# Kernel tuning notes

Hardware: AMD Instinct MI355X
Metric: run time of the kernel (lower is better)

## Reference

```python
import jax, jax.numpy as jnp
import numpy as np

B, T, D, H, L = 64, 4096, 128, 128, 2


def setup_inputs() -> dict:
    key = jax.random.key(0)
    ks = jax.random.split(key, 9)
    s = 1.0 / np.sqrt(H)
    return {
        "x": jax.random.normal(ks[0], (B, T, D), dtype=jnp.float32),
        "W_ih0": jax.random.normal(ks[1], (3 * H, D), dtype=jnp.float32) * s,
        "W_hh0": jax.random.normal(ks[2], (3 * H, H), dtype=jnp.float32) * s,
        "b_ih0": jax.random.normal(ks[3], (3 * H,), dtype=jnp.float32) * s,
        "b_hh0": jax.random.normal(ks[4], (3 * H,), dtype=jnp.float32) * s,
        "W_ih1": jax.random.normal(ks[5], (3 * H, H), dtype=jnp.float32) * s,
        "W_hh1": jax.random.normal(ks[6], (3 * H, H), dtype=jnp.float32) * s,
        "b_ih1": jax.random.normal(ks[7], (3 * H,), dtype=jnp.float32) * s,
        "b_hh1": jax.random.normal(ks[8], (3 * H,), dtype=jnp.float32) * s,
    }


def _gru_cell(h, xt, W_ih, W_hh, b_ih, b_hh):
    # torch.nn.GRUCell math; gates packed as [r, z, n] along 3H.
    gi = xt @ W_ih.T + b_ih            # [B, 3H]
    gh = h @ W_hh.T + b_hh             # [B, 3H]
    i_r, i_z, i_n = jnp.split(gi, 3, axis=-1)
    h_r, h_z, h_n = jnp.split(gh, 3, axis=-1)
    r = jax.nn.sigmoid(i_r + h_r)
    z = jax.nn.sigmoid(i_z + h_z)
    n = jnp.tanh(i_n + r * h_n)
    return (1.0 - z) * n + z * h


def reference(x, W_ih0, W_hh0, b_ih0, b_hh0, W_ih1, W_hh1, b_ih1, b_hh1):
    h0 = jnp.zeros((L, x.shape[0], H), dtype=x.dtype)
    params = ((W_ih0, W_hh0, b_ih0, b_hh0), (W_ih1, W_hh1, b_ih1, b_hh1))

    def step(h, xt):
        # h: [L, B, H]; xt: [B, D]
        inp = xt
        new_h = []
        for l in range(L):
            hl = _gru_cell(h[l], inp, *params[l])
            new_h.append(hl)
            inp = hl
        return jnp.stack(new_h, axis=0), None

    xs = jnp.swapaxes(x, 0, 1)  # [T, B, D]
    h_final, _ = jax.lax.scan(step, h0, xs)
    return h_final  # [L, B, H]
```

## Files before the change

### kernel.cpp

```cpp
#include <hip/hip_runtime.h>


#define Tlen 4096
#define Hd   128
#define Bsz  64

typedef __attribute__((ext_vector_type(8))) short short8;
typedef __attribute__((ext_vector_type(4))) short short4v;
typedef __attribute__((ext_vector_type(4))) float float4v;
typedef __attribute__((ext_vector_type(2))) unsigned int uint2v;

#define MFMA16(a, b, c) __builtin_amdgcn_mfma_f32_16x16x32_bf16((a), (b), (c), 0, 0, 0)

static __device__ __forceinline__ float fast_exp2(float x) {
#if __has_builtin(__builtin_amdgcn_exp2f)
  return __builtin_amdgcn_exp2f(x);
#else
  return exp2f(x);
#endif
}
static __device__ __forceinline__ float fast_rcp(float x) {
  return __builtin_amdgcn_rcpf(x);
}
static __device__ __forceinline__ short f2bf(float f) {
  unsigned u = __builtin_bit_cast(unsigned, f);
  u = (u + 0x7FFFu + ((u >> 16) & 1u)) >> 16;
  return (short)u;
}
static __device__ __forceinline__ unsigned pk2bf(float a, float b) {
#if __has_builtin(__builtin_amdgcn_cvt_pk_bf16_f32)
  auto v = __builtin_amdgcn_cvt_pk_bf16_f32(a, b);
  return __builtin_bit_cast(unsigned, v);
#else
  return (unsigned)(unsigned short)f2bf(a) | ((unsigned)(unsigned short)f2bf(b) << 16);
#endif
}
static __device__ __forceinline__ short8 loadw8(const float* __restrict__ p) {
  short8 r;
  #pragma unroll
  for (int j = 0; j < 8; ++j) r[j] = f2bf(p[j]);
  return r;
}

#define XB   0
#define H0B  4096
#define H1B  8192
#define BLK  2048

__global__ __launch_bounds__(512, 2) void gru_scan(
    const float* __restrict__ x,
    const float* __restrict__ Wih0, const float* __restrict__ Whh0,
    const float* __restrict__ bih0, const float* __restrict__ bhh0,
    const float* __restrict__ Wih1, const float* __restrict__ Whh1,
    const float* __restrict__ bih1, const float* __restrict__ bhh1,
    float* __restrict__ out) {
  __shared__ alignas(16) short Abuf[12288];

  const int tid   = threadIdx.x;
  const int wave  = tid >> 6;
  const int lane  = tid & 63;
  const int lc    = lane & 15;
  const int quad  = lane >> 4;
  const int q8    = quad * 8;
  const int lane8 = lane * 8;
  const int bbase = blockIdx.x * 16;

  const int wgrp = wave >> 2;
  const int w4   = wave & 3;

  const float* Wi = wgrp ? Wih1 : Wih0;
  const float* Wh = wgrp ? Whh1 : Whh0;
  const float* bi = wgrp ? bih1 : bih0;
  const float* bh = wgrp ? bhh1 : bhh0;

  short8 fxr[2][4], fxz[2][4], fxn[2][4];
  short8 fhr[2][4], fhz[2][4], fhn[2][4];
  float kr[2], kz[2], ki[2], kh[2];
  const float nL  = -1.44269504088896f;
  const float n2L = -2.88539008177793f;
  #pragma unroll
  for (int G = 0; G < 2; ++G) {
    const int c = 32 * w4 + 16 * G + lc;
    #pragma unroll
    for (int s = 0; s < 4; ++s) {
      const int k = 32 * s + q8;
      fxr[G][s] = loadw8(Wi + (c)       * Hd + k);
      fxz[G][s] = loadw8(Wi + (128 + c) * Hd + k);
      fxn[G][s] = loadw8(Wi + (256 + c) * Hd + k);
      fhr[G][s] = loadw8(Wh + (c)       * Hd + k);
      fhz[G][s] = loadw8(Wh + (128 + c) * Hd + k);
      fhn[G][s] = loadw8(Wh + (256 + c) * Hd + k);
    }
    kr[G] = nL  * (bi[c] + bh[c]);
    kz[G] = nL  * (bi[128 + c] + bh[128 + c]);
    ki[G] = n2L * bi[256 + c];
    kh[G] = n2L * bh[256 + c];
  }

  const int hsel = wgrp ? H1B : H0B;
  const int isel = wgrp ? H0B : XB;

  int hw[2];
  #pragma unroll
  for (int G = 0; G < 2; ++G)
    hw[G] = w4 * 512 + (2 * G + (lc >> 3)) * 128 + (lc & 7);

  const int xrow = tid >> 5;
  const int xk0  = 4 * (tid & 31);
  const int xwoff = (xk0 >> 5) * 512 + ((xk0 >> 3) & 3) * 128 + xrow * 8 + (xk0 & 7);
  const float* xg = x + (size_t)(bbase + xrow) * (Tlen * Hd) + xk0;

  const int glo = wgrp ? 2 : 0;
  const int ghi = glo + Tlen;

  {
    int* zb = (int*)Abuf;
    #pragma unroll
    for (int i = 0; i < 8; ++i) zb[2048 + tid + 512 * i] = 0;
    const float4v v0 = *(const float4v*)(xg);
    const float4v v1 = *(const float4v*)(xg + Hd);
    uint2v p0 = {pk2bf(v0[0], v0[1]), pk2bf(v0[2], v0[3])};
    uint2v p1 = {pk2bf(v1[0], v1[1]), pk2bf(v1[2], v1[3])};
    *(short4v*)&Abuf[XB + xwoff]       = __builtin_bit_cast(short4v, p0);
    *(short4v*)&Abuf[XB + BLK + xwoff] = __builtin_bit_cast(short4v, p1);
  }
  __syncthreads();

  const float4v Z4 = {0.f, 0.f, 0.f, 0.f};
  float4v ar[2], az[2], an[2], ah[2];
  float4v hp[2] = {Z4, Z4};

  #pragma unroll
  for (int G = 0; G < 2; ++G) { ar[G] = Z4; az[G] = Z4; an[G] = Z4; ah[G] = Z4; }
  #pragma unroll
  for (int s = 0; s < 4; ++s) {
    const short8 a = *(const short8*)&Abuf[isel + s * 512 + lane8];
    #pragma unroll
    for (int G = 0; G < 2; ++G) {
      ar[G] = MFMA16(a, fxr[G][s], ar[G]);
      az[G] = MFMA16(a, fxz[G][s], az[G]);
      an[G] = MFMA16(a, fxn[G][s], an[G]);
    }
  }

  for (int t = 0; t < Tlen + 2; ++t) {
    const int par  = (t & 1) * BLK;
    const int parx = BLK - par;

    const int tn = (t + 2 < Tlen) ? (t + 2) : (Tlen - 1);
    const float4v xv = *(const float4v*)(xg + (size_t)tn * Hd);
    const int hrd = hsel + parx;
    #pragma unroll
    for (int s = 0; s < 4; ++s) {
      const short8 a = *(const short8*)&Abuf[hrd + s * 512 + lane8];
      #pragma unroll
      for (int G = 0; G < 2; ++G) {
        ar[G] = MFMA16(a, fhr[G][s], ar[G]);
        az[G] = MFMA16(a, fhz[G][s], az[G]);
        ah[G] = MFMA16(a, fhn[G][s], ah[G]);
      }
    }
    if (t >= glo && t < ghi) {
      const int wr = hsel + par;
      #pragma unroll
      for (int G = 0; G < 2; ++G) {
        #pragma unroll
        for (int i = 0; i < 4; ++i) {
          const float er = fast_exp2(fmaf(ar[G][i], nL, kr[G]));
          const float rr = fast_rcp(1.0f + er);
          const float ez = fast_exp2(fmaf(az[G][i], nL, kz[G]));
          const float zz = fast_rcp(1.0f + ez);
          float vv = fmaf(rr, fmaf(ah[G][i], n2L, kh[G]),
                          fmaf(an[G][i], n2L, ki[G]));
          vv = fminf(vv, 126.0f);
          const float e2 = fast_exp2(vv);
          const float nn = (1.0f - e2) * fast_rcp(1.0f + e2);
          const float hn = fmaf(zz, hp[G][i] - nn, nn);
          hp[G][i] = hn;
          Abuf[wr + hw[G] + (quad * 4 + i) * 8] = f2bf(hn);
        }
      }
    }
    __syncthreads();

    {
      uint2v pp = {pk2bf(xv[0], xv[1]), pk2bf(xv[2], xv[3])};
      *(short4v*)&Abuf[XB + par + xwoff] = __builtin_bit_cast(short4v, pp);
    }
    const int ird = isel + parx;
    #pragma unroll
    for (int G = 0; G < 2; ++G) { ar[G] = Z4; az[G] = Z4; an[G] = Z4; ah[G] = Z4; }
    #pragma unroll
    for (int s = 0; s < 4; ++s) {
      const short8 a = *(const short8*)&Abuf[ird + s * 512 + lane8];
      #pragma unroll
      for (int G = 0; G < 2; ++G) {
        ar[G] = MFMA16(a, fxr[G][s], ar[G]);
        az[G] = MFMA16(a, fxz[G][s], az[G]);
        an[G] = MFMA16(a, fxn[G][s], an[G]);
      }
    }
    __syncthreads();
  }

  #pragma unroll
  for (int G = 0; G < 2; ++G) {
    const int u = 32 * w4 + 16 * G + lc;
    #pragma unroll
    for (int i = 0; i < 4; ++i) {
      const int b = bbase + quad * 4 + i;
      out[wgrp * (Bsz * Hd) + b * Hd + u] = hp[G][i];
    }
  }
}

extern "C" void kernel_launch(void* const* d_in, const int* in_sizes, int n_in,
                              void* d_out, int out_size, void* d_ws, size_t ws_size,
                              hipStream_t stream) {
  (void)in_sizes; (void)n_in; (void)out_size; (void)d_ws; (void)ws_size;
  gru_scan<<<4, 512, 0, stream>>>(
      (const float*)d_in[0],
      (const float*)d_in[1], (const float*)d_in[2],
      (const float*)d_in[3], (const float*)d_in[4],
      (const float*)d_in[5], (const float*)d_in[6],
      (const float*)d_in[7], (const float*)d_in[8],
      (float*)d_out);
}
```

Measured before the change: 8.688 ms.

## Split GRU layers across workgroups with global-memory FIFO and flag handshakes

Moves from 4 workgroups that each run both layers to 8 workgroups, one per layer and batch block. Layer 0 streams its hidden states through a 16-deep ring buffer in global memory, and layer 1 consumes them, with acquire/release flags providing producer-consumer sync and backpressure. Each wave now computes one 16-column group instead of two, which halves the serial MFMA and gate work per step and spreads it over more CUs. In exchange it adds cross-workgroup polling latency, global-memory traffic, and relies on all 8 blocks being co-resident to avoid deadlock.

```diff
diff --git a/kernel.cpp b/kernel.cpp
--- a/kernel.cpp
+++ b/kernel.cpp
@@ -1,9 +1,10 @@
 #include <hip/hip_runtime.h>
 
 
-#define Tlen 4096
-#define Hd   128
-#define Bsz  64
+#define Tlen  4096
+#define Hd    128
+#define Bsz   64
+#define DEPTH 16
 
 typedef __attribute__((ext_vector_type(8))) short short8;
 typedef __attribute__((ext_vector_type(4))) short short4v;
@@ -41,10 +42,15 @@
   for (int j = 0; j < 8; ++j) r[j] = f2bf(p[j]);
   return r;
 }
-
-#define XB   0
-#define H0B  4096
-#define H1B  8192
+static __device__ __forceinline__ int flag_acq(const int* p) {
+  return __hip_atomic_load(p, __ATOMIC_ACQUIRE, __HIP_MEMORY_SCOPE_AGENT);
+}
+static __device__ __forceinline__ void flag_rel(int* p, int v) {
+  __hip_atomic_store(p, v, __ATOMIC_RELEASE, __HIP_MEMORY_SCOPE_AGENT);
+}
+
+#define HB   0
+#define INB  4096
 #define BLK  2048
 
 __global__ __launch_bounds__(512, 2) void gru_scan(
@@ -53,8 +59,9 @@
     const float* __restrict__ bih0, const float* __restrict__ bhh0,
     const float* __restrict__ Wih1, const float* __restrict__ Whh1,
     const float* __restrict__ bih1, const float* __restrict__ bhh1,
-    float* __restrict__ out) {
-  __shared__ alignas(16) short Abuf[12288];
+    float* __restrict__ out, int* __restrict__ flags,
+    short* __restrict__ fifo) {
+  __shared__ alignas(16) short Abuf[8192];
 
   const int tid   = threadIdx.x;
   const int wave  = tid >> 6;
@@ -63,166 +70,173 @@
   const int quad  = lane >> 4;
   const int q8    = quad * 8;
   const int lane8 = lane * 8;
-  const int bbase = blockIdx.x * 16;
-
-  const int wgrp = wave >> 2;
-  const int w4   = wave & 3;
-
-  const float* Wi = wgrp ? Wih1 : Wih0;
-  const float* Wh = wgrp ? Whh1 : Whh0;
-  const float* bi = wgrp ? bih1 : bih0;
-  const float* bh = wgrp ? bhh1 : bhh0;
-
-  short8 fxr[2][4], fxz[2][4], fxn[2][4];
-  short8 fhr[2][4], fhz[2][4], fhn[2][4];
-  float kr[2], kz[2], ki[2], kh[2];
+  const int rb    = blockIdx.x & 3;
+  const int lyr   = blockIdx.x >> 2;
+  const int bbase = rb * 16;
+
+  const float* Wi = lyr ? Wih1 : Wih0;
+  const float* Wh = lyr ? Whh1 : Whh0;
+  const float* bi = lyr ? bih1 : bih0;
+  const float* bh = lyr ? bhh1 : bhh0;
+
+  short8 fxr[4], fxz[4], fxn[4];
+  short8 fhr[4], fhz[4], fhn[4];
   const float nL  = -1.44269504088896f;
   const float n2L = -2.88539008177793f;
-  #pragma unroll
-  for (int G = 0; G < 2; ++G) {
-    const int c = 32 * w4 + 16 * G + lc;
-    #pragma unroll
-    for (int s = 0; s < 4; ++s) {
-      const int k = 32 * s + q8;
-      fxr[G][s] = loadw8(Wi + (c)       * Hd + k);
-      fxz[G][s] = loadw8(Wi + (128 + c) * Hd + k);
-      fxn[G][s] = loadw8(Wi + (256 + c) * Hd + k);
-      fhr[G][s] = loadw8(Wh + (c)       * Hd + k);
-      fhz[G][s] = loadw8(Wh + (128 + c) * Hd + k);
-      fhn[G][s] = loadw8(Wh + (256 + c) * Hd + k);
-    }
-    kr[G] = nL  * (bi[c] + bh[c]);
-    kz[G] = nL  * (bi[128 + c] + bh[128 + c]);
-    ki[G] = n2L * bi[256 + c];
-    kh[G] = n2L * bh[256 + c];
-  }
-
-  const int hsel = wgrp ? H1B : H0B;
-  const int isel = wgrp ? H0B : XB;
-
-  int hw[2];
-  #pragma unroll
-  for (int G = 0; G < 2; ++G)
-    hw[G] = w4 * 512 + (2 * G + (lc >> 3)) * 128 + (lc & 7);
-
-  const int xrow = tid >> 5;
-  const int xk0  = 4 * (tid & 31);
-  const int xwoff = (xk0 >> 5) * 512 + ((xk0 >> 3) & 3) * 128 + xrow * 8 + (xk0 & 7);
-  const float* xg = x + (size_t)(bbase + xrow) * (Tlen * Hd) + xk0;
-
-  const int glo = wgrp ? 2 : 0;
-  const int ghi = glo + Tlen;
+  const int c = 16 * wave + lc;
+  #pragma unroll
+  for (int s = 0; s < 4; ++s) {
+    const int k = 32 * s + q8;
+    fxr[s] = loadw8(Wi + (c)       * Hd + k);
+    fxz[s] = loadw8(Wi + (128 + c) * Hd + k);
+    fxn[s] = loadw8(Wi + (256 + c) * Hd + k);
+    fhr[s] = loadw8(Wh + (c)       * Hd + k);
+    fhz[s] = loadw8(Wh + (128 + c) * Hd + k);
+    fhn[s] = loadw8(Wh + (256 + c) * Hd + k);
+  }
+  const float kr = nL  * (bi[c] + bh[c]);
+  const float kz = nL  * (bi[128 + c] + bh[128 + c]);
+  const float ki = n2L * bi[256 + c];
+  const float kh = n2L * bh[256 + c];
+
+  const int hwb = (wave >> 1) * 512 + ((wave & 1) * 2 + (lc >> 3)) * 128 + (lc & 7);
+
+  const int srow  = tid >> 5;
+  const int sk0   = 4 * (tid & 31);
+  const int swoff = (sk0 >> 5) * 512 + ((sk0 >> 3) & 3) * 128 + srow * 8 + (sk0 & 7);
+  const float* xg = x + (size_t)(bbase + srow) * (Tlen * Hd) + sk0;
+
+  short* fifo_rb = fifo + (size_t)rb * (DEPTH * BLK);
+  int* d0 = flags + rb;
+  int* d1 = flags + 4 + rb;
 
   {
     int* zb = (int*)Abuf;
     #pragma unroll
-    for (int i = 0; i < 8; ++i) zb[2048 + tid + 512 * i] = 0;
-    const float4v v0 = *(const float4v*)(xg);
-    const float4v v1 = *(const float4v*)(xg + Hd);
-    uint2v p0 = {pk2bf(v0[0], v0[1]), pk2bf(v0[2], v0[3])};
-    uint2v p1 = {pk2bf(v1[0], v1[1]), pk2bf(v1[2], v1[3])};
-    *(short4v*)&Abuf[XB + xwoff]       = __builtin_bit_cast(short4v, p0);
-    *(short4v*)&Abuf[XB + BLK + xwoff] = __builtin_bit_cast(short4v, p1);
+    for (int i = 0; i < 4; ++i) zb[tid + 512 * i] = 0;
+    if (lyr == 0) {
+      const float4v v0 = *(const float4v*)(xg);
+      const float4v v1 = *(const float4v*)(xg + Hd);
+      uint2v p0 = {pk2bf(v0[0], v0[1]), pk2bf(v0[2], v0[3])};
+      uint2v p1 = {pk2bf(v1[0], v1[1]), pk2bf(v1[2], v1[3])};
+      *(short4v*)&Abuf[INB + swoff]       = __builtin_bit_cast(short4v, p0);
+      *(short4v*)&Abuf[INB + BLK + swoff] = __builtin_bit_cast(short4v, p1);
+    } else {
+      while (flag_acq(d0) < 1) __builtin_amdgcn_s_sleep(8);
+      const short4v h0a = *(const short4v*)(fifo_rb + 0 * BLK + srow * 128 + sk0);
+      const short4v h0b = *(const short4v*)(fifo_rb + 1 * BLK + srow * 128 + sk0);
+      *(short4v*)&Abuf[INB + swoff]       = h0a;
+      *(short4v*)&Abuf[INB + BLK + swoff] = h0b;
+    }
   }
   __syncthreads();
 
   const float4v Z4 = {0.f, 0.f, 0.f, 0.f};
-  float4v ar[2], az[2], an[2], ah[2];
-  float4v hp[2] = {Z4, Z4};
-
-  #pragma unroll
-  for (int G = 0; G < 2; ++G) { ar[G] = Z4; az[G] = Z4; an[G] = Z4; ah[G] = Z4; }
+  float4v ar = Z4, az = Z4, an = Z4, ah = Z4;
+  float4v hp = Z4;
+
   #pragma unroll
   for (int s = 0; s < 4; ++s) {
-    const short8 a = *(const short8*)&Abuf[isel + s * 512 + lane8];
-    #pragma unroll
-    for (int G = 0; G < 2; ++G) {
-      ar[G] = MFMA16(a, fxr[G][s], ar[G]);
-      az[G] = MFMA16(a, fxz[G][s], az[G]);
-      an[G] = MFMA16(a, fxn[G][s], an[G]);
-    }
-  }
-
-  for (int t = 0; t < Tlen + 2; ++t) {
+    const short8 a = *(const short8*)&Abuf[INB + s * 512 + lane8];
+    ar = MFMA16(a, fxr[s], ar);
+    az = MFMA16(a, fxz[s], az);
+    an = MFMA16(a, fxn[s], an);
+  }
+
+  for (int t = 0; t < Tlen; ++t) {
     const int par  = (t & 1) * BLK;
     const int parx = BLK - par;
-
-    const int tn = (t + 2 < Tlen) ? (t + 2) : (Tlen - 1);
-    const float4v xv = *(const float4v*)(xg + (size_t)tn * Hd);
-    const int hrd = hsel + parx;
+    const int tn   = (t + 2 < Tlen) ? (t + 2) : (Tlen - 1);
+
+    float4v xv;
+    short4v hv;
+    int fd = 0x7fffffff;
+    if (lyr == 0) {
+      xv = *(const float4v*)(xg + (size_t)tn * Hd);
+      if ((t & 3) == 0) fd = flag_acq(d1);
+      if ((t & 1) == 0 && t > 0 && tid == 0) flag_rel(d0, t - 1);
+    } else {
+      fd = flag_acq(d0);
+      if ((t & 3) == 0 && tid == 0) flag_rel(d1, t + 1);
+    }
+    const int hrd = HB + parx;
     #pragma unroll
     for (int s = 0; s < 4; ++s) {
       const short8 a = *(const short8*)&Abuf[hrd + s * 512 + lane8];
+      ar = MFMA16(a, fhr[s], ar);
+      az = MFMA16(a, fhz[s], az);
+      ah = MFMA16(a, fhn[s], ah);
+    }
+    if (lyr == 0) {
+      if ((t & 3) == 0) {
+        while (fd < t - 13) { __builtin_amdgcn_s_sleep(8); fd = flag_acq(d1); }
+      }
+    } else {
+      while (fd < tn) { __builtin_amdgcn_s_sleep(8); fd = flag_acq(d0); }
+      hv = *(const short4v*)(fifo_rb + (size_t)(tn & (DEPTH - 1)) * BLK +
+                             srow * 128 + sk0);
+    }
+    __syncthreads();
+
+    {
+      const int wr = HB + par;
+      const int fw = (t & (DEPTH - 1)) * BLK;
       #pragma unroll
-      for (int G = 0; G < 2; ++G) {
-        ar[G] = MFMA16(a, fhr[G][s], ar[G]);
-        az[G] = MFMA16(a, fhz[G][s], az[G]);
-        ah[G] = MFMA16(a, fhn[G][s], ah[G]);
+      for (int i = 0; i < 4; ++i) {
+        const float er = fast_exp2(fmaf(ar[i], nL, kr));
+        const float rr = fast_rcp(1.0f + er);
+        const float ez = fast_exp2(fmaf(az[i], nL, kz));
+        const float zz = fast_rcp(1.0f + ez);
+        float vv = fmaf(rr, fmaf(ah[i], n2L, kh), fmaf(an[i], n2L, ki));
+        vv = fminf(vv, 126.0f);
+        const float e2 = fast_exp2(vv);
+        const float nn = (1.0f - e2) * fast_rcp(1.0f + e2);
+        const float hn = fmaf(zz, hp[i] - nn, nn);
+        hp[i] = hn;
+        const short hb = f2bf(hn);
+        Abuf[wr + hwb + (quad * 4 + i) * 8] = hb;
+        if (lyr == 0) fifo_rb[fw + (quad * 4 + i) * 128 + c] = hb;
       }
     }
-    if (t >= glo && t < ghi) {
-      const int wr = hsel + par;
-      #pragma unroll
-      for (int G = 0; G < 2; ++G) {
-        #pragma unroll
-        for (int i = 0; i < 4; ++i) {
-          const float er = fast_exp2(fmaf(ar[G][i], nL, kr[G]));
-          const float rr = fast_rcp(1.0f + er);
-          const float ez = fast_exp2(fmaf(az[G][i], nL, kz[G]));
-          const float zz = fast_rcp(1.0f + ez);
-          float vv = fmaf(rr, fmaf(ah[G][i], n2L, kh[G]),
-                          fmaf(an[G][i], n2L, ki[G]));
-          vv = fminf(vv, 126.0f);
-          const float e2 = fast_exp2(vv);
-          const float nn = (1.0f - e2) * fast_rcp(1.0f + e2);
-          const float hn = fmaf(zz, hp[G][i] - nn, nn);
-          hp[G][i] = hn;
-          Abuf[wr + hw[G] + (quad * 4 + i) * 8] = f2bf(hn);
-        }
+    {
+      if (lyr == 0) {
+        uint2v pp = {pk2bf(xv[0], xv[1]), pk2bf(xv[2], xv[3])};
+        *(short4v*)&Abuf[INB + par + swoff] = __builtin_bit_cast(short4v, pp);
+      } else {
+        *(short4v*)&Abuf[INB + par + swoff] = hv;
       }
     }
-    __syncthreads();
-
-    {
-      uint2v pp = {pk2bf(xv[0], xv[1]), pk2bf(xv[2], xv[3])};
-      *(short4v*)&Abuf[XB + par + xwoff] = __builtin_bit_cast(short4v, pp);
-    }
-    const int ird = isel + parx;
-    #pragma unroll
-    for (int G = 0; G < 2; ++G) { ar[G] = Z4; az[G] = Z4; an[G] = Z4; ah[G] = Z4; }
+    const int ird = INB + parx;
+    ar = Z4; az = Z4; an = Z4; ah = Z4;
     #pragma unroll
     for (int s = 0; s < 4; ++s) {
       const short8 a = *(const short8*)&Abuf[ird + s * 512 + lane8];
-      #pragma unroll
-      for (int G = 0; G < 2; ++G) {
-        ar[G] = MFMA16(a, fxr[G][s], ar[G]);
-        az[G] = MFMA16(a, fxz[G][s], az[G]);
-        an[G] = MFMA16(a, fxn[G][s], an[G]);
-      }
+      ar = MFMA16(a, fxr[s], ar);
+      az = MFMA16(a, fxz[s], az);
+      an = MFMA16(a, fxn[s], an);
     }
     __syncthreads();
   }
 
-  #pragma unroll
-  for (int G = 0; G < 2; ++G) {
-    const int u = 32 * w4 + 16 * G + lc;
-    #pragma unroll
-    for (int i = 0; i < 4; ++i) {
-      const int b = bbase + quad * 4 + i;
-      out[wgrp * (Bsz * Hd) + b * Hd + u] = hp[G][i];
-    }
+  if (lyr == 0 && tid == 0) flag_rel(d0, Tlen - 1);
+
+  #pragma unroll
+  for (int i = 0; i < 4; ++i) {
+    const int b = bbase + quad * 4 + i;
+    out[lyr * (Bsz * Hd) + b * Hd + c] = hp[i];
   }
 }
 
 extern "C" void kernel_launch(void* const* d_in, const int* in_sizes, int n_in,
                               void* d_out, int out_size, void* d_ws, size_t ws_size,
                               hipStream_t stream) {
-  (void)in_sizes; (void)n_in; (void)out_size; (void)d_ws; (void)ws_size;
-  gru_scan<<<4, 512, 0, stream>>>(
+  (void)in_sizes; (void)n_in; (void)out_size; (void)ws_size;
+  hipMemsetAsync(d_ws, 0xFF, 64, stream);
+  gru_scan<<<8, 512, 0, stream>>>(
       (const float*)d_in[0],
       (const float*)d_in[1], (const float*)d_in[2],
       (const float*)d_in[3], (const float*)d_in[4],
       (const float*)d_in[5], (const float*)d_in[6],
       (const float*)d_in[7], (const float*)d_in[8],
-      (float*)d_out);
-}
+      (float*)d_out, (int*)d_ws, (short*)((char*)d_ws + 256));
+}
```

Result: faster. 7.428 ms (-14.5%).
